# Performance work log

Measured on AMD Instinct MI355X. Metric: run time of the kernel, lower is better.

The kernel has to match this reference:

```python
import jax, jax.numpy as jnp
import numpy as np

N_SAMPLES_DEPTHS = [64, 32, 16]
DEPTH_RES_LEVELS = [2, 2, 2]
NV = 3
IMG_H = IMG_W = 512
VOL = 128


def trilinear_lookup(vol, pts):
    """Trilinear sample of vol[D,H,W] at pts[...,3] in [-1,1] (x->W, y->H, z->D).
    Matches F.grid_sample(mode='bilinear', padding_mode='border', align_corners=True)."""
    D, H, W = vol.shape
    x = jnp.clip((pts[..., 0] + 1.0) * 0.5 * (W - 1), 0.0, W - 1.0)
    y = jnp.clip((pts[..., 1] + 1.0) * 0.5 * (H - 1), 0.0, H - 1.0)
    z = jnp.clip((pts[..., 2] + 1.0) * 0.5 * (D - 1), 0.0, D - 1.0)
    x0f = jnp.floor(x); y0f = jnp.floor(y); z0f = jnp.floor(z)
    wx = x - x0f; wy = y - y0f; wz = z - z0f
    x0 = x0f.astype(jnp.int32); y0 = y0f.astype(jnp.int32); z0 = z0f.astype(jnp.int32)
    x1 = jnp.minimum(x0 + 1, W - 1)
    y1 = jnp.minimum(y0 + 1, H - 1)
    z1 = jnp.minimum(z0 + 1, D - 1)
    c000 = vol[z0, y0, x0]; c001 = vol[z0, y0, x1]
    c010 = vol[z0, y1, x0]; c011 = vol[z0, y1, x1]
    c100 = vol[z1, y0, x0]; c101 = vol[z1, y0, x1]
    c110 = vol[z1, y1, x0]; c111 = vol[z1, y1, x1]
    c00 = c000 * (1 - wx) + c001 * wx
    c01 = c010 * (1 - wx) + c011 * wx
    c10 = c100 * (1 - wx) + c101 * wx
    c11 = c110 * (1 - wx) + c111 * wx
    c0 = c00 * (1 - wy) + c01 * wy
    c1 = c10 * (1 - wy) + c11 * wy
    return c0 * (1 - wz) + c1 * wz


def _make_c2w(angle):
    c, s = np.cos(angle), np.sin(angle)
    m = np.eye(4, dtype=np.float32)
    m[:3, :3] = np.array([[c, 0, s], [0, 1, 0], [-s, 0, c]], np.float32)
    m[:3, 3] = np.array([0.3 * np.sin(angle), 0.0, -1.5], np.float32)
    return m


def setup_inputs() -> dict:
    key = jax.random.key(0)
    k_img, k_vol = jax.random.split(key)
    imgs = jax.random.normal(k_img, (NV, 3, IMG_H, IMG_W), dtype=jnp.float32)
    f = 400.0
    intr = np.array([[f, 0.0, IMG_W / 2], [0.0, f, IMG_H / 2], [0.0, 0.0, 1.0]], np.float32)
    intrs = jnp.asarray(np.stack([intr] * NV))
    c2ws = jnp.asarray(np.stack([_make_c2w(a) for a in (0.0, 0.15, -0.15)]))
    near_fars = jnp.tile(jnp.array([[0.5, 3.0]], jnp.float32), (NV, 1))
    density_volume = jax.random.normal(k_vol, (VOL, VOL, VOL), dtype=jnp.float32)
    return {"imgs": imgs, "intrs": intrs, "c2ws": c2ws, "near_fars": near_fars,
            "density_volume": density_volume, "stage_idx": 0}


def reference(imgs, intrs, c2ws, near_fars, density_volume, stage_idx):
    img_h, img_w = imgs.shape[-2:]
    res = DEPTH_RES_LEVELS[stage_idx]
    h, w = img_h // res, img_w // res
    n_s = N_SAMPLES_DEPTHS[stage_idx]

    # pixel grid at reduced resolution (matches torch.meshgrid 'ij')
    ty = jnp.linspace(0.0, img_h - 1.0, h)
    tx = jnp.linspace(0.0, img_w - 1.0, w)
    py, px = jnp.meshgrid(ty, tx, indexing='ij')
    pixels = jnp.stack([px.reshape(-1), py.reshape(-1), jnp.ones(h * w, jnp.float32)], -1)  # [N,3]
    t_lin = jnp.linspace(0.0, 1.0, n_s)  # [S]

    def render_view(c2w, intr, near_far):
        cam = pixels @ jnp.linalg.inv(intr).T                      # [N,3]
        rays_d = cam / jnp.linalg.norm(cam, axis=-1, keepdims=True)
        rays_d = rays_d @ c2w[:3, :3].T                            # world-space dirs
        z_vals = near_far[0] + (near_far[1] - near_far[0]) * t_lin  # [S] (single stage: already sorted)
        pts = c2w[None, None, :3, 3] + rays_d[:, None, :] * z_vals[None, :, None]  # [N,S,3]
        outside = jax.lax.stop_gradient((jnp.linalg.norm(pts, axis=-1) > 1.0).astype(pts.dtype))  # [N,S]
        density = trilinear_lookup(density_volume, pts)            # [N,S]
        weights = jax.nn.softmax(density, axis=-1)
        cam_rays_d = rays_d @ jnp.linalg.inv(c2w[:3, :3]).T        # back to camera frame
        render_z = jnp.sum(z_vals[None, :] * weights, axis=1)      # [N]
        render_depth = (render_z * cam_rays_d[:, 2]).reshape(h, w)
        occ_reg = density[:, :6].mean() + (density * outside).sum() / (outside.sum() + 1e-10)
        depth_full = jax.image.resize(render_depth, (img_h, img_w), method='bilinear')
        return depth_full, occ_reg

    depths, occs = jax.vmap(render_view)(c2ws, intrs, near_fars)
    # views other than src_idx=0 are rendered under no_grad in the original
    depths = jnp.concatenate([depths[:1], jax.lax.stop_gradient(depths[1:])], axis=0)
    occs = jnp.concatenate([occs[:1], jax.lax.stop_gradient(occs[1:])], axis=0)
    return depths, occs
```

## Files before the change

kernel.cpp:

```cpp
#include <hip/hip_runtime.h>
#include <hip/hip_fp16.h>
#include <math.h>

#define NVIEW 3
#define HLOW 256
#define WLOW 256
#define NPIX (HLOW * WLOW)
#define NS 64
#define VOLN 128
#define IMGH 512
#define IMGW 512
#define BLK 256
#define BLOCKS_PER_VIEW (NPIX / BLK)
#define NVOX (VOLN * VOLN * VOLN)
#define UPS2_BLOCKS ((NVIEW * IMGH * IMGW / 2) / BLK)
#define NXCD 8
#define MARCH_BLOCKS (NVIEW * BLOCKS_PER_VIEW)
#define CHUNK (MARCH_BLOCKS / NXCD)

#define LOG2E     1.4426950408889634f
#define INV_LOG2E 0.6931471805599453f

typedef _Float16 h2 __attribute__((ext_vector_type(2)));

struct Ray {
    float ax0, axs, ay0, ays, az0, azs;
    float sLo, sHi;
    float z0, zstep, ncz;
};

__device__ __forceinline__ Ray ray_setup(
    int view, int row, int col,
    const float* __restrict__ intrs, const float* __restrict__ c2ws,
    const float* __restrict__ nf)
{
    const float px = 511.0f * (float)col * (1.0f / 255.0f);
    const float py = 511.0f * (float)row * (1.0f / 255.0f);

    const float* K = intrs + view * 9;
    const float a = K[0], b = K[1], c = K[2];
    const float d = K[3], e = K[4], f = K[5];
    const float g = K[6], h = K[7], i9 = K[8];
    const float det = a * (e * i9 - f * h) - b * (d * i9 - f * g) + c * (d * h - e * g);
    const float id = 1.0f / det;
    const float m00 = (e * i9 - f * h) * id, m01 = -(b * i9 - c * h) * id, m02 = (b * f - c * e) * id;
    const float m10 = -(d * i9 - f * g) * id, m11 = (a * i9 - c * g) * id, m12 = -(a * f - c * d) * id;
    const float m20 = (d * h - e * g) * id, m21 = -(a * h - b * g) * id, m22 = (a * e - b * d) * id;

    const float cx = m00 * px + m01 * py + m02;
    const float cy = m10 * px + m11 * py + m12;
    const float cz = m20 * px + m21 * py + m22;
    const float inr = rsqrtf(cx * cx + cy * cy + cz * cz);
    const float ncz = cz * inr;

    const float ncx = cx * inr, ncy = cy * inr;
    const float* M = c2ws + view * 16;
    const float dx = M[0] * ncx + M[1] * ncy + M[2] * ncz;
    const float dy = M[4] * ncx + M[5] * ncy + M[6] * ncz;
    const float dz = M[8] * ncx + M[9] * ncy + M[10] * ncz;
    const float tx = M[3], ty = M[7], tz = M[11];

    const float z0 = nf[view * 2 + 0];
    const float zstep = (nf[view * 2 + 1] - z0) * (1.0f / 63.0f);

    Ray r;
    const float gx0 = (tx + 1.0f) * 63.5f, gxs = dx * 63.5f;
    const float gy0 = (ty + 1.0f) * 63.5f, gys = dy * 63.5f;
    const float gz0 = (tz + 1.0f) * 63.5f, gzs = dz * 63.5f;
    r.ax0 = fmaf(gxs, z0, gx0); r.axs = gxs * zstep;
    r.ay0 = fmaf(gys, z0, gy0); r.ays = gys * zstep;
    r.az0 = fmaf(gzs, z0, gz0); r.azs = gzs * zstep;

    const float bq = tx * dx + ty * dy + tz * dz;
    const float cq = tx * tx + ty * ty + tz * tz;
    const float disc = bq * bq - (cq - 1.0f);
    if (disc >= 0.0f) {
        const float rt = sqrtf(disc);
        const float inv = 1.0f / zstep;
        r.sLo = (-bq - rt - z0) * inv;
        r.sHi = (-bq + rt - z0) * inv;
    } else {
        r.sLo = 3.4e38f;
        r.sHi = 0.0f;
    }

    r.z0 = z0;
    r.zstep = zstep;
    r.ncz = ncz;
    return r;
}

__global__ __launch_bounds__(BLK) void build_quad_kernel(
    const float* __restrict__ vol, uint4* __restrict__ F)
{
    const int id = blockIdx.x * BLK + threadIdx.x;
    const int x = id & 127;
    const int y = (id >> 7) & 127;
    const int z = id >> 14;
    const int yp = min(y + 1, 127);
    const int zp = min(z + 1, 127);
    const int xb = min(x, 126);
    const int sel = x - xb;

    const float2 v00 = *reinterpret_cast<const float2*>(vol + (z  * VOLN + y ) * VOLN + xb);
    const float2 v01 = *reinterpret_cast<const float2*>(vol + (z  * VOLN + yp) * VOLN + xb);
    const float2 v10 = *reinterpret_cast<const float2*>(vol + (zp * VOLN + y ) * VOLN + xb);
    const float2 v11 = *reinterpret_cast<const float2*>(vol + (zp * VOLN + yp) * VOLN + xb);

    const float c000 = sel ? v00.y : v00.x, c001 = v00.y;
    const float c010 = sel ? v01.y : v01.x, c011 = v01.y;
    const float c100 = sel ? v10.y : v10.x, c101 = v10.y;
    const float c110 = sel ? v11.y : v11.x, c111 = v11.y;

    const __half2 w0 = __floats2half2_rn(c000 * LOG2E, c100 * LOG2E);
    const __half2 w1 = __floats2half2_rn(c001 * LOG2E, c101 * LOG2E);
    const __half2 w2 = __floats2half2_rn(c010 * LOG2E, c110 * LOG2E);
    const __half2 w3 = __floats2half2_rn(c011 * LOG2E, c111 * LOG2E);
    uint4 o;
    o.x = *reinterpret_cast<const unsigned*>(&w0);
    o.y = *reinterpret_cast<const unsigned*>(&w1);
    o.z = *reinterpret_cast<const unsigned*>(&w2);
    o.w = *reinterpret_cast<const unsigned*>(&w3);
    F[id] = o;
}

__global__ __launch_bounds__(BLK) void raymarch_quad_kernel(
    const float* __restrict__ intrs, const float* __restrict__ c2ws,
    const float* __restrict__ nf, const uint4* __restrict__ F,
    float* __restrict__ depth_low, float* __restrict__ partials)
{
    const int wg  = blockIdx.x;
    const int swz = (wg & (NXCD - 1)) * CHUNK + (wg >> 3);
    const int view = swz >> 8;
    const int row  = swz & 255;
    const int t    = threadIdx.x;

    const Ray r = ray_setup(view, row, t, intrs, c2ws, nf);

    const float ilo = ceilf(fmaxf(r.sLo, 0.0f));
    const float ihi = floorf(fminf(r.sHi, 63.0f));
    const float cnt = 64.0f - fmaxf(0.0f, ihi - ilo + 1.0f);

    float lsum = 0.0f, sacc = 0.0f, d6 = 0.0f, dout = 0.0f;

    h2 fx2[2][8], fy2[2][8], fw2[2][8];
    uint4 q[2][8];

#define ADDR_BATCH(BK, SB)                                                    \
    {                                                                         \
        unsigned offs[8];                                                     \
        _Pragma("unroll")                                                     \
        for (int i = 0; i < 8; ++i) {                                         \
            const float sf = (float)((SB) + i);                               \
            float gx = fmaf(r.axs, sf, r.ax0);                                \
            float gy = fmaf(r.ays, sf, r.ay0);                                \
            float gz = fmaf(r.azs, sf, r.az0);                                \
            gx = fminf(fmaxf(gx, 0.0f), 126.9995f);                           \
            gy = fminf(fmaxf(gy, 0.0f), 126.9995f);                           \
            gz = fminf(fmaxf(gz, 0.0f), 126.9995f);                           \
            const float xbf = floorf(gx);                                     \
            const float ybf = floorf(gy);                                     \
            const float zbf = floorf(gz);                                     \
            const float fx = gx - xbf;                                        \
            const float fy = gy - ybf;                                        \
            const float fz = gz - zbf;                                        \
            fx2[BK][i] = (h2){(_Float16)fx, (_Float16)fx};                    \
            fy2[BK][i] = (h2){(_Float16)fy, (_Float16)fy};                    \
            fw2[BK][i] = (h2){(_Float16)(1.0f - fz), (_Float16)fz};           \
            offs[i] = (unsigned)fmaf(zbf, 16384.0f, fmaf(ybf, 128.0f, xbf));  \
        }                                                                     \
        _Pragma("unroll")                                                     \
        for (int i = 0; i < 8; ++i) q[BK][i] = F[offs[i]];                    \
    }

#define CONSUME_BATCH(BK, SB)                                                 \
    _Pragma("unroll")                                                         \
    for (int i = 0; i < 8; ++i) {                                             \
        const float sf = (float)((SB) + i);                                   \
        const h2 a0 = __builtin_bit_cast(h2, q[BK][i].x);                     \
        const h2 a1 = __builtin_bit_cast(h2, q[BK][i].y);                     \
        const h2 b0 = __builtin_bit_cast(h2, q[BK][i].z);                     \
        const h2 b1 = __builtin_bit_cast(h2, q[BK][i].w);                     \
        const h2 cx0 = fx2[BK][i] * (a1 - a0) + a0;             \
        const h2 cx1 = fx2[BK][i] * (b1 - b0) + b0;                           \
        const h2 cyv = fy2[BK][i] * (cx1 - cx0) + cx0;                        \
        const float dens =                                                    \
            __builtin_amdgcn_fdot2(cyv, fw2[BK][i], 0.0f, false);             \
        const float w = exp2f(dens);                             \
        lsum += w;                                                            \
        sacc = fmaf(sf, w, sacc);                                             \
        if ((SB) == 0 && i < 6) d6 += dens;                                   \
        const bool o = (sf < r.sLo) || (sf > r.sHi);                          \
        dout += o ? dens : 0.0f;                                              \
    }

    ADDR_BATCH(0, 0)
    #pragma unroll
    for (int b = 0; b < 8; ++b) {
        if (b < 7) {
            if (b & 1) { ADDR_BATCH(0, (b + 1) * 8) }
            else       { ADDR_BATCH(1, (b + 1) * 8) }
        }
        if (b & 1) { CONSUME_BATCH(1, b * 8) }
        else       { CONSUME_BATCH(0, b * 8) }
    }
#undef ADDR_BATCH
#undef CONSUME_BATCH

    depth_low[view * NPIX + row * WLOW + t] =
        fmaf(r.zstep, sacc / lsum, r.z0) * r.ncz;

    __shared__ float s0[BLK], s1[BLK], s2[BLK];
    s0[t] = d6; s1[t] = dout; s2[t] = cnt;
    __syncthreads();
    for (int off = BLK / 2; off > 0; off >>= 1) {
        if (t < off) {
            s0[t] += s0[t + off];
            s1[t] += s1[t + off];
            s2[t] += s2[t + off];
        }
        __syncthreads();
    }
    if (t == 0) {
        partials[swz * 3 + 0] = s0[0] * INV_LOG2E;
        partials[swz * 3 + 1] = s1[0] * INV_LOG2E;
        partials[swz * 3 + 2] = s2[0];
    }
}

__global__ __launch_bounds__(BLK) void raymarch_f32_kernel(
    const float* __restrict__ intrs, const float* __restrict__ c2ws,
    const float* __restrict__ nf, const float* __restrict__ vol,
    float* __restrict__ depth_low, float* __restrict__ partials)
{
    const int view = blockIdx.x >> 8;
    const int row  = blockIdx.x & 255;
    const int t    = threadIdx.x;

    const Ray r = ray_setup(view, row, t, intrs, c2ws, nf);

    const float ilo = ceilf(fmaxf(r.sLo, 0.0f));
    const float ihi = floorf(fminf(r.sHi, 63.0f));
    const float cnt = 64.0f - fmaxf(0.0f, ihi - ilo + 1.0f);

    float lsum = 0.0f, sacc = 0.0f, d6 = 0.0f, dout = 0.0f;

    #pragma unroll 16
    for (int s = 0; s < NS; ++s) {
        const float sf = (float)s;
        float gx = fmaf(r.axs, sf, r.ax0);
        float gy = fmaf(r.ays, sf, r.ay0);
        float gz = fmaf(r.azs, sf, r.az0);
        gx = fminf(fmaxf(gx, 0.0f), 126.9995f);
        gy = fminf(fmaxf(gy, 0.0f), 126.9995f);
        gz = fminf(fmaxf(gz, 0.0f), 126.9995f);
        const float xbf = floorf(gx);
        const float ybf = floorf(gy);
        const float zbf = floorf(gz);
        const float fx = gx - xbf, fy = gy - ybf, fz = gz - zbf;
        const unsigned off = (unsigned)fmaf(zbf, 16384.0f, fmaf(ybf, 128.0f, xbf));

        const float* p0 = vol + off;
        const float2 v00 = *reinterpret_cast<const float2*>(p0);
        const float2 v01 = *reinterpret_cast<const float2*>(p0 + VOLN);
        const float2 v10 = *reinterpret_cast<const float2*>(p0 + VOLN * VOLN);
        const float2 v11 = *reinterpret_cast<const float2*>(p0 + VOLN * VOLN + VOLN);

        const float c00 = fmaf(fx, v00.y - v00.x, v00.x);
        const float c01 = fmaf(fx, v01.y - v01.x, v01.x);
        const float c10 = fmaf(fx, v10.y - v10.x, v10.x);
        const float c11 = fmaf(fx, v11.y - v11.x, v11.x);
        const float c0 = fmaf(fy, c01 - c00, c00);
        const float c1 = fmaf(fy, c11 - c10, c10);
        const float dens = fmaf(fz, c1 - c0, c0);

        const float w = __expf(dens);
        lsum += w;
        sacc = fmaf(sf, w, sacc);

        if (s < 6) d6 += dens;
        const bool o = (sf < r.sLo) || (sf > r.sHi);
        dout += o ? dens : 0.0f;
    }

    depth_low[view * NPIX + row * WLOW + t] =
        fmaf(r.zstep, sacc / lsum, r.z0) * r.ncz;

    __shared__ float s0[BLK], s1[BLK], s2[BLK];
    s0[t] = d6; s1[t] = dout; s2[t] = cnt;
    __syncthreads();
    for (int off = BLK / 2; off > 0; off >>= 1) {
        if (t < off) {
            s0[t] += s0[t + off];
            s1[t] += s1[t + off];
            s2[t] += s2[t + off];
        }
        __syncthreads();
    }
    if (t == 0) {
        partials[blockIdx.x * 3 + 0] = s0[0];
        partials[blockIdx.x * 3 + 1] = s1[0];
        partials[blockIdx.x * 3 + 2] = s2[0];
    }
}

__global__ __launch_bounds__(BLK) void epilogue_kernel(
    const float* __restrict__ low, const float* __restrict__ partials,
    float* __restrict__ out)
{
    if (blockIdx.x >= UPS2_BLOCKS) {
        const int view = blockIdx.x - UPS2_BLOCKS;
        const int t = threadIdx.x;
        __shared__ float s0[BLK], s1[BLK], s2[BLK];
        const int bi = view * BLOCKS_PER_VIEW + t;
        s0[t] = partials[bi * 3 + 0];
        s1[t] = partials[bi * 3 + 1];
        s2[t] = partials[bi * 3 + 2];
        __syncthreads();
        for (int off = BLK / 2; off > 0; off >>= 1) {
            if (t < off) {
                s0[t] += s0[t + off];
                s1[t] += s1[t + off];
                s2[t] += s2[t + off];
            }
            __syncthreads();
        }
        if (t == 0) {
            out[NVIEW * IMGH * IMGW + view] =
                s0[0] * (1.0f / (float)(NPIX * 6)) + s1[0] / (s2[0] + 1e-10f);
        }
        return;
    }

    const int idx2 = blockIdx.x * BLK + threadIdx.x;
    const int view = idx2 / (IMGH * IMGW / 2);
    const int rem  = idx2 - view * (IMGH * IMGW / 2);
    const int rr = rem >> 8;
    const int cp = rem & 255;
    const int cc0 = cp * 2;

    const float sy = (float)rr * 0.5f - 0.25f;
    const float y0f = floorf(sy);
    const float wy = sy - y0f;
    const int y0 = (int)y0f;
    const int y0c = max(y0, 0), y1c = min(y0 + 1, HLOW - 1);
    const float* src = low + view * NPIX;
    const float* r0 = src + y0c * WLOW;
    const float* r1 = src + y1c * WLOW;

    float2 res;
    {
        const float sx = (float)cc0 * 0.5f - 0.25f;
        const float x0f = floorf(sx);
        const float wx = sx - x0f;
        const int x0 = (int)x0f;
        const int x0c = max(x0, 0), x1c = min(x0 + 1, WLOW - 1);
        const float top = r0[x0c] * (1.0f - wx) + r0[x1c] * wx;
        const float bot = r1[x0c] * (1.0f - wx) + r1[x1c] * wx;
        res.x = top * (1.0f - wy) + bot * wy;
    }
    {
        const int cc1 = cc0 + 1;
        const float sx = (float)cc1 * 0.5f - 0.25f;
        const float x0f = floorf(sx);
        const float wx = sx - x0f;
        const int x0 = (int)x0f;
        const int x0c = max(x0, 0), x1c = min(x0 + 1, WLOW - 1);
        const float top = r0[x0c] * (1.0f - wx) + r0[x1c] * wx;
        const float bot = r1[x0c] * (1.0f - wx) + r1[x1c] * wx;
        res.y = top * (1.0f - wy) + bot * wy;
    }
    *reinterpret_cast<float2*>(out + view * (IMGH * IMGW) + rr * IMGW + cc0) = res;
}

extern "C" void kernel_launch(void* const* d_in, const int* in_sizes, int n_in,
                              void* d_out, int out_size, void* d_ws, size_t ws_size,
                              hipStream_t stream) {
    const float* intrs = (const float*)d_in[1];
    const float* c2ws  = (const float*)d_in[2];
    const float* nf    = (const float*)d_in[3];
    const float* vol   = (const float*)d_in[4];
    float* out = (float*)d_out;

    const size_t quad_bytes  = (size_t)NVOX * 16;
    const size_t depth_bytes = (size_t)NVIEW * NPIX * 4;
    const size_t part_bytes  = (size_t)NVIEW * BLOCKS_PER_VIEW * 3 * 4;
    char* ws = (char*)d_ws;

    float* depth_low;
    float* partials;

    if (ws_size >= quad_bytes + depth_bytes + part_bytes) {
        uint4* F = (uint4*)ws;
        depth_low = (float*)(ws + quad_bytes);
        partials  = depth_low + NVIEW * NPIX;
        build_quad_kernel<<<NVOX / BLK, BLK, 0, stream>>>(vol, F);
        raymarch_quad_kernel<<<MARCH_BLOCKS, BLK, 0, stream>>>(
            intrs, c2ws, nf, F, depth_low, partials);
    } else {
        depth_low = (float*)ws;
        partials  = depth_low + NVIEW * NPIX;
        raymarch_f32_kernel<<<MARCH_BLOCKS, BLK, 0, stream>>>(
            intrs, c2ws, nf, vol, depth_low, partials);
    }

    epilogue_kernel<<<UPS2_BLOCKS + NVIEW, BLK, 0, stream>>>(depth_low, partials, out);
}
```

Before: 37.33 us.

## Pack volume as 8-byte YZ-corner pairs and read overlapping 16-byte spans

Replaces the 16-byte-per-voxel precomputed trilinear corner table with an 8-byte-per-voxel table holding the four (y,z) corners in fp16. The march kernel reads 16 bytes starting at voxel x, which covers voxels x and x+1 and so yields all eight corners. Interpolation changes to fp16 lerp in x, a dot2 over y weights, then an fp32 lerp in z. This halves the table's footprint and build writes, improving cache hit rates. In exchange the loads are only 8-byte aligned, and the z lerp now runs in fp32 with two dot2 ops.

After: 34.72 us, median of 2. 7.0% less time.

```diff
diff --git a/kernel.cpp b/kernel.cpp
--- a/kernel.cpp
+++ b/kernel.cpp
@@ -90,8 +90,8 @@
     return r;
 }
 
-__global__ __launch_bounds__(BLK) void build_quad_kernel(
-    const float* __restrict__ vol, uint4* __restrict__ F)
+__global__ __launch_bounds__(BLK) void build_pack8_kernel(
+    const float* __restrict__ vol, uint2* __restrict__ P)
 {
     const int id = blockIdx.x * BLK + threadIdx.x;
     const int x = id & 127;
@@ -99,34 +99,23 @@
     const int z = id >> 14;
     const int yp = min(y + 1, 127);
     const int zp = min(z + 1, 127);
-    const int xb = min(x, 126);
-    const int sel = x - xb;
-
-    const float2 v00 = *reinterpret_cast<const float2*>(vol + (z  * VOLN + y ) * VOLN + xb);
-    const float2 v01 = *reinterpret_cast<const float2*>(vol + (z  * VOLN + yp) * VOLN + xb);
-    const float2 v10 = *reinterpret_cast<const float2*>(vol + (zp * VOLN + y ) * VOLN + xb);
-    const float2 v11 = *reinterpret_cast<const float2*>(vol + (zp * VOLN + yp) * VOLN + xb);
-
-    const float c000 = sel ? v00.y : v00.x, c001 = v00.y;
-    const float c010 = sel ? v01.y : v01.x, c011 = v01.y;
-    const float c100 = sel ? v10.y : v10.x, c101 = v10.y;
-    const float c110 = sel ? v11.y : v11.x, c111 = v11.y;
-
-    const __half2 w0 = __floats2half2_rn(c000 * LOG2E, c100 * LOG2E);
-    const __half2 w1 = __floats2half2_rn(c001 * LOG2E, c101 * LOG2E);
-    const __half2 w2 = __floats2half2_rn(c010 * LOG2E, c110 * LOG2E);
-    const __half2 w3 = __floats2half2_rn(c011 * LOG2E, c111 * LOG2E);
-    uint4 o;
+
+    const float v00 = vol[(z  * VOLN + y ) * VOLN + x];
+    const float v01 = vol[(z  * VOLN + yp) * VOLN + x];
+    const float v10 = vol[(zp * VOLN + y ) * VOLN + x];
+    const float v11 = vol[(zp * VOLN + yp) * VOLN + x];
+
+    const __half2 w0 = __floats2half2_rn(v00 * LOG2E, v01 * LOG2E);
+    const __half2 w1 = __floats2half2_rn(v10 * LOG2E, v11 * LOG2E);
+    uint2 o;
     o.x = *reinterpret_cast<const unsigned*>(&w0);
     o.y = *reinterpret_cast<const unsigned*>(&w1);
-    o.z = *reinterpret_cast<const unsigned*>(&w2);
-    o.w = *reinterpret_cast<const unsigned*>(&w3);
-    F[id] = o;
-}
-
-__global__ __launch_bounds__(BLK) void raymarch_quad_kernel(
+    P[id] = o;
+}
+
+__global__ __launch_bounds__(BLK) void raymarch_pack8_kernel(
     const float* __restrict__ intrs, const float* __restrict__ c2ws,
-    const float* __restrict__ nf, const uint4* __restrict__ F,
+    const float* __restrict__ nf, const char* __restrict__ Fb,
     float* __restrict__ depth_low, float* __restrict__ partials)
 {
     const int wg  = blockIdx.x;
@@ -143,7 +132,8 @@
 
     float lsum = 0.0f, sacc = 0.0f, d6 = 0.0f, dout = 0.0f;
 
-    h2 fx2[2][8], fy2[2][8], fw2[2][8];
+    h2 fx2[2][8], fyw[2][8];
+    float fzs[2][8];
     uint4 q[2][8];
 
 #define ADDR_BATCH(BK, SB)                                                    \
@@ -163,29 +153,29 @@
             const float zbf = floorf(gz);                                     \
             const float fx = gx - xbf;                                        \
             const float fy = gy - ybf;                                        \
-            const float fz = gz - zbf;                                        \
+            fzs[BK][i] = gz - zbf;                                            \
             fx2[BK][i] = (h2){(_Float16)fx, (_Float16)fx};                    \
-            fy2[BK][i] = (h2){(_Float16)fy, (_Float16)fy};                    \
-            fw2[BK][i] = (h2){(_Float16)(1.0f - fz), (_Float16)fz};           \
+            fyw[BK][i] = (h2){(_Float16)(1.0f - fy), (_Float16)fy};           \
             offs[i] = (unsigned)fmaf(zbf, 16384.0f, fmaf(ybf, 128.0f, xbf));  \
         }                                                                     \
         _Pragma("unroll")                                                     \
-        for (int i = 0; i < 8; ++i) q[BK][i] = F[offs[i]];                    \
+        for (int i = 0; i < 8; ++i)                                           \
+            q[BK][i] = *reinterpret_cast<const uint4*>(Fb + (size_t)offs[i] * 8); \
     }
 
 #define CONSUME_BATCH(BK, SB)                                                 \
     _Pragma("unroll")                                                         \
     for (int i = 0; i < 8; ++i) {                                             \
         const float sf = (float)((SB) + i);                                   \
-        const h2 a0 = __builtin_bit_cast(h2, q[BK][i].x);                     \
-        const h2 a1 = __builtin_bit_cast(h2, q[BK][i].y);                     \
-        const h2 b0 = __builtin_bit_cast(h2, q[BK][i].z);                     \
-        const h2 b1 = __builtin_bit_cast(h2, q[BK][i].w);                     \
-        const h2 cx0 = fx2[BK][i] * (a1 - a0) + a0;             \
-        const h2 cx1 = fx2[BK][i] * (b1 - b0) + b0;                           \
-        const h2 cyv = fy2[BK][i] * (cx1 - cx0) + cx0;                        \
-        const float dens =                                                    \
-            __builtin_amdgcn_fdot2(cyv, fw2[BK][i], 0.0f, false);             \
+        const h2 w0 = __builtin_bit_cast(h2, q[BK][i].x);                     \
+        const h2 w1 = __builtin_bit_cast(h2, q[BK][i].y);                     \
+        const h2 w2 = __builtin_bit_cast(h2, q[BK][i].z);                     \
+        const h2 w3 = __builtin_bit_cast(h2, q[BK][i].w);                     \
+        const h2 cx0 = fx2[BK][i] * (w2 - w0) + w0;          \
+        const h2 cx1 = fx2[BK][i] * (w3 - w1) + w1;          \
+        const float c0 = __builtin_amdgcn_fdot2(cx0, fyw[BK][i], 0.0f, false);\
+        const float c1 = __builtin_amdgcn_fdot2(cx1, fyw[BK][i], 0.0f, false);\
+        const float dens = fmaf(fzs[BK][i], c1 - c0, c0);      \
         const float w = exp2f(dens);                             \
         lsum += w;                                                            \
         sacc = fmaf(sf, w, sacc);                                             \
@@ -382,7 +372,7 @@
     const float* vol   = (const float*)d_in[4];
     float* out = (float*)d_out;
 
-    const size_t quad_bytes  = (size_t)NVOX * 16;
+    const size_t pack_bytes  = (size_t)NVOX * 8 + 16;
     const size_t depth_bytes = (size_t)NVIEW * NPIX * 4;
     const size_t part_bytes  = (size_t)NVIEW * BLOCKS_PER_VIEW * 3 * 4;
     char* ws = (char*)d_ws;
@@ -390,13 +380,13 @@
     float* depth_low;
     float* partials;
 
-    if (ws_size >= quad_bytes + depth_bytes + part_bytes) {
-        uint4* F = (uint4*)ws;
-        depth_low = (float*)(ws + quad_bytes);
+    if (ws_size >= pack_bytes + depth_bytes + part_bytes) {
+        uint2* P = (uint2*)ws;
+        depth_low = (float*)(ws + pack_bytes);
         partials  = depth_low + NVIEW * NPIX;
-        build_quad_kernel<<<NVOX / BLK, BLK, 0, stream>>>(vol, F);
-        raymarch_quad_kernel<<<MARCH_BLOCKS, BLK, 0, stream>>>(
-            intrs, c2ws, nf, F, depth_low, partials);
+        build_pack8_kernel<<<NVOX / BLK, BLK, 0, stream>>>(vol, P);
+        raymarch_pack8_kernel<<<MARCH_BLOCKS, BLK, 0, stream>>>(
+            intrs, c2ws, nf, (const char*)ws, depth_low, partials);
     } else {
         depth_low = (float*)ws;
         partials  = depth_low + NVIEW * NPIX;
```
